# Optimization experiments

Hardware: AMD Instinct MI355X
Metric: run time of the kernel (lower is better)

Reference implementation:

```python
import jax, jax.numpy as jnp
import numpy as np

K = 20
EPS = 1e-5
N = 4096


def lrelu(x):
    return jnp.where(x >= 0, x, 0.2 * x)


def bn(x, g, b, m, v):
    # eval-mode BatchNorm over channel dim 1
    shape = [1] * x.ndim
    shape[1] = -1
    inv = g / jnp.sqrt(v + EPS)
    return (x - m.reshape(shape)) * inv.reshape(shape) + b.reshape(shape)


def get_graph_feature(x):
    # Faithful to repo: num_points = x.shape[1], remaining dims fold into channels.
    p = x.shape[1]
    x2d = x.reshape(-1, p)              # (C, P)
    xx = jnp.sum(x2d * x2d, axis=0)     # (P,)
    dist = 2.0 * (x2d.T @ x2d) - xx[:, None] - xx[None, :]  # -||xi-xj||^2, (P, P)
    idx = jax.lax.top_k(dist, K)[1]     # (P, K) nearest neighbors (incl. self)
    xt = x2d.T                          # (P, C)
    feat = xt[idx]                      # (P, K, C) neighbor gather
    ctr = jnp.broadcast_to(xt[:, None, :], feat.shape)
    out = jnp.concatenate([feat - ctr, ctr], axis=-1)  # (P, K, 2C)
    return out.transpose(2, 0, 1)[None]                # (1, 2C, P, K)


def setup_inputs():
    key = jax.random.key(0)
    ks = jax.random.split(key, 16)

    def w(k_, o, c):
        return jax.random.normal(k_, (o, c), jnp.float32) / float(np.sqrt(c))

    def bnp(k_, c):
        k1, k2, k3, k4 = jax.random.split(k_, 4)
        return (1.0 + 0.1 * jax.random.normal(k1, (c,), jnp.float32),
                0.1 * jax.random.normal(k2, (c,), jnp.float32),
                0.1 * jax.random.normal(k3, (c,), jnp.float32),
                jax.random.uniform(k4, (c,), jnp.float32, minval=0.5, maxval=1.5))

    g1, b1, m1, v1 = bnp(ks[1], 64)
    g2, b2, m2, v2 = bnp(ks[2], 64)
    g3, b3, m3, v3 = bnp(ks[3], 128)
    g4, b4, m4, v4 = bnp(ks[4], 256)
    g5, b5, m5, v5 = bnp(ks[5], 512)
    return dict(
        x=jax.random.normal(ks[0], (3, N), jnp.float32),
        w1=w(ks[6], 64, 6), g1=g1, b1=b1, m1=m1, v1=v1,
        w2=w(ks[7], 64, 64), g2=g2, b2=b2, m2=m2, v2=v2,
        w3=w(ks[8], 128, 64), g3=g3, b3=b3, m3=m3, v3=v3,
        w4=w(ks[9], 256, 128), g4=g4, b4=b4, m4=m4, v4=v4,
        w5=w(ks[10], 512, 256), g5=g5, b5=b5, m5=m5, v5=v5,
        lw1=w(ks[11], 512, 1024),
        lw2=w(ks[12], 256, 512),
        lb2=0.1 * jax.random.normal(ks[13], (256,), jnp.float32),
        ow=w(ks[14], 11, 256),
        ob=0.1 * jax.random.normal(ks[15], (11,), jnp.float32),
    )


def reference(x, w1, g1, b1, m1, v1, w2, g2, b2, m2, v2, w3, g3, b3, m3, v3,
              w4, g4, b4, m4, v4, w5, g5, b5, m5, v5, lw1, lw2, lb2, ow, ob):
    conv2d = lambda w_, f_: jnp.einsum('oc,bcpk->bopk', w_, f_)

    f = get_graph_feature(x)                                   # (1, 6, N, K)
    h = lrelu(bn(conv2d(w1, f), g1, b1, m1, v1))
    x1 = jnp.max(h, axis=-1)                                   # (1, 64, N)

    f = jnp.swapaxes(get_graph_feature(x1), 1, 2)              # (1, 64, 2N, K)
    h = lrelu(bn(conv2d(w2, f), g2, b2, m2, v2))
    x2 = jnp.max(h, axis=-1)                                   # (1, 64, 2N)

    f = jnp.swapaxes(get_graph_feature(x2), 1, 2)              # (1, 64, 4N, K)
    h = lrelu(bn(conv2d(w3, f), g3, b3, m3, v3))
    x3 = jnp.max(h, axis=-1)                                   # (1, 128, 4N)

    f = jnp.swapaxes(get_graph_feature(x3), 1, 2)              # (1, 128, 8N, K)
    h = lrelu(bn(conv2d(w4, f), g4, b4, m4, v4))
    x4 = jnp.max(h, axis=-1)                                   # (1, 256, 8N)

    h5 = lrelu(bn(jnp.einsum('oc,bcp->bop', w5, x4), g5, b5, m5, v5))  # (1, 512, 8N)
    pmax = jnp.max(h5, axis=-1)
    pavg = jnp.mean(h5, axis=-1)
    z = jnp.concatenate([pmax, pavg], axis=1)                  # (1, 1024)
    z = lrelu(z @ lw1.T)                                       # (1, 512); dropout = eval identity
    z = lrelu(z @ lw2.T + lb2)                                 # (1, 256)
    logits = z @ ow.T + ob                                     # (1, 11)
    return jax.nn.softmax(logits, axis=1)
```

## Files before the change

### kernel.cpp

```cpp
#include <hip/hip_runtime.h>
#include <hip/hip_bf16.h>
#include <float.h>
#include <math.h>

#define DEV __device__ __forceinline__

DEV float lrelu(float x) { return x >= 0.f ? x : 0.2f * x; }

constexpr int N = 4096, KNN = 20;

typedef __attribute__((ext_vector_type(4))) float f32x4;
typedef __attribute__((ext_vector_type(8))) short s16x8;

constexpr size_t OFF_SC1 = 0,    OFF_SH1 = 64;
constexpr size_t OFF_SC2 = 128,  OFF_SH2 = 192;
constexpr size_t OFF_SC3 = 256,  OFF_SH3 = 384;
constexpr size_t OFF_SC4 = 512,  OFF_SH4 = 768;
constexpr size_t OFF_SC5 = 1024, OFF_SH5 = 1536;
constexpr size_t OFF_X1 = 2048;
constexpr size_t OFF_X2 = OFF_X1 + (size_t)64*4096;
constexpr size_t OFF_X3 = OFF_X2 + (size_t)64*8192;
constexpr size_t OFF_X4 = OFF_X3 + (size_t)128*16384;
constexpr size_t OFF_A  = OFF_X4 + (size_t)256*32768;
constexpr size_t OFF_GP = OFF_A + (size_t)256*21*128;
constexpr size_t OFF_PM = OFF_GP + (size_t)64*128*128;
constexpr size_t OFF_PS = OFF_PM + (size_t)512*256;
constexpr size_t OFF_Z0 = OFF_PS + (size_t)512*256;
constexpr size_t OFF_Z1 = OFF_Z0 + 1024;
constexpr size_t OFF_Z2 = OFF_Z1 + 512;
constexpr size_t OFF_IDX = OFF_Z2 + 256;
constexpr size_t WS_NEEDED_BYTES = OFF_IDX * 4 + (size_t)N * KNN * 4;
constexpr size_t OFF_ABF = OFF_A;
constexpr size_t OFF_W5BF = OFF_A + 524288;

__global__ void k_ws_sentinel(float* out, float mb) {
  int t = threadIdx.x;
  if (t < 11) out[t] = 1.0e6f + mb;
}

__global__ __launch_bounds__(512) void k_bn_pre(
    const float* g1, const float* b1, const float* m1, const float* v1,
    const float* g2, const float* b2, const float* m2, const float* v2,
    const float* g3, const float* b3, const float* m3, const float* v3,
    const float* g4, const float* b4, const float* m4, const float* v4,
    const float* g5, const float* b5, const float* m5, const float* v5,
    float* ws) {
  int t = threadIdx.x;
  const float* G[5] = {g1,g2,g3,g4,g5};
  const float* B[5] = {b1,b2,b3,b4,b5};
  const float* M[5] = {m1,m2,m3,m4,m5};
  const float* V[5] = {v1,v2,v3,v4,v5};
  const size_t SC[5] = {OFF_SC1,OFF_SC2,OFF_SC3,OFF_SC4,OFF_SC5};
  const size_t SH[5] = {OFF_SH1,OFF_SH2,OFF_SH3,OFF_SH4,OFF_SH5};
  const int CN[5] = {64,64,128,256,512};
  for (int s = 0; s < 5; ++s) {
    for (int i = t; i < CN[s]; i += 512) {
      float scale = G[s][i] / sqrtf(V[s][i] + 1e-5f);
      ws[SC[s] + i] = scale;
      ws[SH[s] + i] = B[s][i] - M[s][i] * scale;
    }
  }
}

__global__ __launch_bounds__(256) void k_s1_topk(const float* x, int* idx) {
  __shared__ float d[N];
  __shared__ float vsh[256];
  __shared__ int ish[256];
  int i = blockIdx.x, t = threadIdx.x;
  {
    #pragma clang fp contract(off)
    float xi0 = x[i], xi1 = x[N + i], xi2 = x[2*N + i];
    float sqi = xi0*xi0 + xi1*xi1 + xi2*xi2;
    for (int j = t; j < N; j += 256) {
      float xj0 = x[j], xj1 = x[N+j], xj2 = x[2*N+j];
      float sqj = xj0*xj0 + xj1*xj1 + xj2*xj2;
      float p = xi0*xj0 + xi1*xj1 + xi2*xj2;
      d[j] = (2.f*p - sqi) - sqj;
    }
  }
  __syncthreads();
  for (int k = 0; k < KNN; ++k) {
    float bv = -FLT_MAX; int bi = N;
    for (int j = t; j < N; j += 256) { float v = d[j]; if (v > bv) { bv = v; bi = j; } }
    vsh[t] = bv; ish[t] = bi;
    __syncthreads();
    for (int s = 128; s > 0; s >>= 1) {
      if (t < s) {
        float v2 = vsh[t+s]; int i2 = ish[t+s];
        if (v2 > vsh[t] || (v2 == vsh[t] && i2 < ish[t])) { vsh[t] = v2; ish[t] = i2; }
      }
      __syncthreads();
    }
    if (t == 0) { idx[i*KNN + k] = ish[0]; d[ish[0]] = -FLT_MAX; }
    __syncthreads();
  }
}

__global__ __launch_bounds__(256) void k_s1_conv(const float* x, const float* w1g,
                                                 const int* idx, const float* sc, const float* sh, float* x1) {
  __shared__ int idxs[64][KNN];
  __shared__ float xs[3][64];
  __shared__ float wsh[4][6];
  int t = threadIdx.x, bx = blockIdx.x, by = blockIdx.y;
  int i0 = bx * 64;
  for (int u = t; u < 64*KNN; u += 256) idxs[u/KNN][u%KNN] = idx[(size_t)(i0 + u/KNN)*KNN + u%KNN];
  for (int u = t; u < 3*64; u += 256) xs[u/64][u%64] = x[(size_t)(u/64)*N + i0 + (u%64)];
  for (int u = t; u < 24; u += 256) wsh[u/6][u%6] = w1g[(size_t)(by*4 + u/6)*6 + u%6];
  __syncthreads();
  int il = t & 63, ol = t >> 6;
  int o = by*4 + ol, i = i0 + il;
  float xi0 = xs[0][il], xi1 = xs[1][il], xi2 = xs[2][il];
  float w0 = wsh[ol][0], w1v = wsh[ol][1], w2v = wsh[ol][2];
  float w3v = wsh[ol][3], w4v = wsh[ol][4], w5v = wsh[ol][5];
  float ctr = w3v*xi0 + w4v*xi1 + w5v*xi2;
  float scale = sc[o], shift = sh[o];
  float best = -FLT_MAX;
  for (int k = 0; k < KNN; ++k) {
    int j = idxs[il][k];
    float h = w0*(x[j] - xi0) + w1v*(x[N+j] - xi1) + w2v*(x[2*N+j] - xi2) + ctr;
    h = lrelu(h*scale + shift);
    best = fmaxf(best, h);
  }
  x1[(size_t)o*N + i] = best;
}

template<int P>
__global__ __launch_bounds__(256) void k_gram_partial(const float* prev, int C, float* gp) {
  constexpr int BI = P / 16;
  __shared__ float ysh[32][P];
  int b = blockIdx.x, t = threadIdx.x;
  int R = C / 64;
  int base = b * R;
  float acc[BI][BI] = {};
  int i0 = (t >> 4) * BI, j0 = (t & 15) * BI;
  for (int r0 = 0; r0 < R; r0 += 32) {
    for (int u = t; u < 32*P; u += 256) ysh[u/P][u%P] = prev[(size_t)(base + r0 + u/P)*P + (u%P)];
    __syncthreads();
    for (int r = 0; r < 32; ++r) {
      float yi[BI], yj[BI];
      #pragma unroll
      for (int a = 0; a < BI; ++a) { yi[a] = ysh[r][i0+a]; yj[a] = ysh[r][j0+a]; }
      #pragma unroll
      for (int a = 0; a < BI; ++a)
        #pragma unroll
        for (int c = 0; c < BI; ++c) acc[a][c] += yi[a]*yj[c];
    }
    __syncthreads();
  }
  for (int a = 0; a < BI; ++a)
    for (int c = 0; c < BI; ++c)
      gp[(size_t)b*P*P + (size_t)(i0+a)*P + (j0+c)] = acc[a][c];
}

template<int P>
__global__ __launch_bounds__(128) void k_dist_topk(const float* gp, int* idx) {
  __shared__ float dsh[P];
  __shared__ float diag[P];
  __shared__ float vsh[128];
  __shared__ int ish[128];
  int i = blockIdx.x, t = threadIdx.x;
  if (t < P) {
    float gij = 0.f, gjj = 0.f;
    for (int b = 0; b < 64; ++b) {
      gij += gp[(size_t)b*P*P + (size_t)i*P + t];
      gjj += gp[(size_t)b*P*P + (size_t)t*P + t];
    }
    diag[t] = gjj;
    dsh[t] = gij;
  }
  __syncthreads();
  if (t < P) dsh[t] = (2.f*dsh[t] - diag[i]) - diag[t];
  __syncthreads();
  for (int k = 0; k < KNN; ++k) {
    float bv = -FLT_MAX; int bi = P;
    if (t < P) { bv = dsh[t]; bi = t; }
    vsh[t] = bv; ish[t] = bi;
    __syncthreads();
    for (int s = 64; s > 0; s >>= 1) {
      if (t < s) {
        float v2 = vsh[t+s]; int i2 = ish[t+s];
        if (v2 > vsh[t] || (v2 == vsh[t] && i2 < ish[t])) { vsh[t] = v2; ish[t] = i2; }
      }
      __syncthreads();
    }
    if (t == 0) { idx[i*KNN + k] = ish[0]; dsh[ish[0]] = -FLT_MAX; }
    __syncthreads();
  }
}

template<int P>
__global__ __launch_bounds__(64) void k_build_A(const float* w, const int* idx, int O, float* A) {
  __shared__ float row[64][P];
  int t = threadIdx.x;
  int r = blockIdx.x*64 + t;
  if (r < O*21) {
    int o = r / 21, kk = r % 21;
    float* my = row[t];
    if (kk == 20) {
      for (int i2 = 0; i2 < P; ++i2) my[i2] = w[(size_t)o*P + i2];
    } else {
      for (int i2 = 0; i2 < P; ++i2) my[i2] = 0.f;
      for (int j = 0; j < P; ++j) my[idx[j*KNN + kk]] += w[(size_t)o*P + j];
    }
    for (int i2 = 0; i2 < P; ++i2) A[(size_t)r*P + i2] = my[i2];
  }
}

__global__ __launch_bounds__(64) void k_build_A_bf(const float* w, const int* idx, __hip_bfloat16* A) {
  __shared__ float row[64][128];
  int t = threadIdx.x;
  int r = blockIdx.x*64 + t;
  int o = r >> 5, kk = r & 31;
  float* my = row[t];
  if (kk == 20) {
    for (int i2 = 0; i2 < 128; ++i2) my[i2] = w[(size_t)o*128 + i2];
  } else if (kk < 20) {
    for (int i2 = 0; i2 < 128; ++i2) my[i2] = 0.f;
    for (int j = 0; j < 128; ++j) my[idx[j*KNN + kk]] += w[(size_t)o*128 + j];
  } else {
    for (int i2 = 0; i2 < 128; ++i2) my[i2] = 0.f;
  }
  for (int i2 = 0; i2 < 128; ++i2) A[(size_t)r*128 + i2] = __float2bfloat16(my[i2]);
}

__global__ __launch_bounds__(256) void k_f32_to_bf16(const float* in, __hip_bfloat16* out) {
  size_t base = ((size_t)blockIdx.x*256 + threadIdx.x) * 16;
  #pragma unroll
  for (int j = 0; j < 4; ++j) {
    float4 v = *(const float4*)(in + base + j*4);
    __hip_bfloat16 tmp[4] = {__float2bfloat16(v.x), __float2bfloat16(v.y),
                             __float2bfloat16(v.z), __float2bfloat16(v.w)};
    *(ushort4*)(out + base + j*4) = *(const ushort4*)tmp;
  }
}

__global__ __launch_bounds__(512, 2) void k_conv4_mfma(const __hip_bfloat16* Abf, const __hip_bfloat16* Xbf,
                                                       const float* sc, const float* sh, float* x4) {
  constexpr int MT = 256;
  __shared__ char Bs[MT*256];
  int t = threadIdx.x, bx = blockIdx.x, byg = blockIdx.y;
  int m0 = bx*MT;
  for (int u = t; u < MT*16; u += 512) {
    int row = u >> 4, k8 = u & 15;
    s16x8 v = *(const s16x8*)(Xbf + ((size_t)(m0+row) << 7) + (k8 << 3));
    *(s16x8*)(Bs + (row << 8) + ((k8 << 4) ^ ((row & 7) << 4))) = v;
  }
  __syncthreads();
  int lane = t & 63, w = t >> 6;
  int col = lane & 15, lg = lane >> 4;
  int q = w & 3, pb = w >> 2;
  for (int it = 0; it < 8; ++it) {
    int by = byg*16 + it*2 + pb;
    const __hip_bfloat16* Ab = Abf + ((size_t)(by*64) << 7);
    f32x4 acc[4][4] = {};
    #pragma unroll
    for (int ks = 0; ks < 4; ++ks) {
      int kel = ks*32 + lg*8;
      int kbyte = ks*64 + lg*16;
      s16x8 a[4], b[4];
      #pragma unroll
      for (int at = 0; at < 4; ++at)
        a[at] = *(const s16x8*)(Ab + ((size_t)(at*16 + col) << 7) + kel);
      #pragma unroll
      for (int bt = 0; bt < 4; ++bt) {
        int r = q*64 + bt*16 + col;
        b[bt] = *(const s16x8*)(Bs + (r << 8) + (kbyte ^ ((r & 7) << 4)));
      }
      #pragma unroll
      for (int at = 0; at < 4; ++at)
        #pragma unroll
        for (int bt = 0; bt < 4; ++bt)
          acc[at][bt] = __builtin_amdgcn_mfma_f32_16x16x32_bf16(a[at], b[bt], acc[at][bt], 0, 0, 0);
    }
    int o0 = by*2;
    #pragma unroll
    for (int ol = 0; ol < 2; ++ol) {
      float scale = sc[o0+ol], shift = sh[o0+ol];
      float mxv[4], ctv[4];
      #pragma unroll
      for (int bt = 0; bt < 4; ++bt) {
        float h2b = __shfl(acc[2*ol+1][bt][0], 16 + col);
        float mx = -FLT_MAX;
        #pragma unroll
        for (int qq = 0; qq < 4; ++qq) {
          mx = fmaxf(mx, lrelu((acc[2*ol][bt][qq] - h2b)*scale + shift));
          float v1 = lrelu((acc[2*ol+1][bt][qq] - h2b)*scale + shift);
          if (lg == 0) mx = fmaxf(mx, v1);
        }
        mx = fmaxf(mx, __shfl_xor(mx, 16));
        mx = fmaxf(mx, __shfl_xor(mx, 32));
        mxv[bt] = mx;
        ctv[bt] = lrelu(h2b*scale + shift);
      }
      float vb = (lg == 0) ? mxv[0] : (lg == 1) ? mxv[1] : (lg == 2) ? mxv[2] : mxv[3];
      float vc = (lg == 0) ? ctv[0] : (lg == 1) ? ctv[1] : (lg == 2) ? ctv[2] : ctv[3];
      size_t pbase = (size_t)(o0+ol)*32768 + m0 + q*64 + lane;
      x4[pbase] = vb;
      x4[pbase + 16384] = vc;
    }
  }
}

template<int P>
__global__ __launch_bounds__(256) void k_fused_conv(const float* prev, const float* A,
                                                    const float* sc, const float* sh,
                                                    int C, float* outx) {
  constexpr int TO = 8, ROWS = TO*21;
  __shared__ float Ash[ROWS][65];
  __shared__ float Bsh[64][132];
  int bx = blockIdx.x, by = blockIdx.y, t = threadIdx.x;
  int m0 = bx*128;
  int rowbase = by*ROWS;
  int ol = t >> 5, mg = t & 31;
  float acc[21][4] = {};
  for (int ic = 0; ic < P/64; ++ic) {
    for (int u = t; u < ROWS*64; u += 256) {
      int rr = u >> 6, cc = u & 63;
      Ash[rr][cc] = A[(size_t)(rowbase + rr)*P + ic*64 + cc];
    }
    for (int u = t; u < 64*128; u += 256) {
      int mr = u >> 6, ii = u & 63;
      Bsh[ii][mr] = prev[(size_t)(m0 + mr)*P + ic*64 + ii];
    }
    __syncthreads();
    for (int i = 0; i < 64; ++i) {
      float v0 = Bsh[i][mg*4+0], v1 = Bsh[i][mg*4+1], v2 = Bsh[i][mg*4+2], v3 = Bsh[i][mg*4+3];
      #pragma unroll
      for (int kk = 0; kk < 21; ++kk) {
        float a = Ash[ol*21 + kk][i];
        acc[kk][0] += a*v0; acc[kk][1] += a*v1; acc[kk][2] += a*v2; acc[kk][3] += a*v3;
      }
    }
    __syncthreads();
  }
  int o = by*TO + ol;
  float scale = sc[o], shift = sh[o];
  size_t C2 = 2*(size_t)C;
  #pragma unroll
  for (int mm = 0; mm < 4; ++mm) {
    int m = m0 + mg*4 + mm;
    float h2 = acc[20][mm];
    float ctr = lrelu(h2*scale + shift);
    float best = -FLT_MAX;
    #pragma unroll
    for (int kk = 0; kk < 20; ++kk) {
      float v = lrelu((acc[kk][mm] - h2)*scale + shift);
      best = fmaxf(best, v);
    }
    outx[(size_t)o*C2 + m] = best;
    outx[(size_t)o*C2 + C + m] = ctr;
  }
}

__global__ __launch_bounds__(256) void k_s5_mfma(const float* x4, const __hip_bfloat16* w5bf,
                                                 const float* sc, const float* sh,
                                                 float* pm, float* ps) {
  __shared__ char smem[8192 + 32768];
  __shared__ float redm[64][4];
  __shared__ float reds[64][4];
  int t = threadIdx.x, bx = blockIdx.x, by = blockIdx.y;
  int p0 = bx*256, o0 = by*64;
  int lane = t & 63, w = t >> 6;
  int lrow = lane & 15, lg = lane >> 4;
  char* As = smem;
  char* Bs = smem + 8192;
  f32x4 acc[4][4] = {};
  for (int c0 = 0; c0 < 256; c0 += 64) {
    for (int u = t; u < 64*8; u += 256) {
      int row = u >> 3, k8 = u & 7;
      s16x8 v = *(const s16x8*)(w5bf + (size_t)(o0+row)*256 + c0 + k8*8);
      *(s16x8*)(As + row*128 + ((k8*16) ^ ((row&7)<<4))) = v;
    }
    #pragma unroll
    for (int i = 0; i < 8; ++i) {
      __hip_bfloat16 tmp[8];
      #pragma unroll
      for (int j = 0; j < 8; ++j)
        tmp[j] = __float2bfloat16(x4[(size_t)(c0 + i*8 + j)*32768 + p0 + t]);
      *(s16x8*)(Bs + t*128 + ((i*16) ^ ((t&7)<<4))) = *(const s16x8*)tmp;
    }
    __syncthreads();
    #pragma unroll
    for (int ksub = 0; ksub < 2; ++ksub) {
      int kbyte = ksub*64 + lg*16;
      s16x8 a[4], b[4];
      #pragma unroll
      for (int rt = 0; rt < 4; ++rt) { int r = rt*16 + lrow; a[rt] = *(const s16x8*)(As + r*128 + (kbyte ^ ((r&7)<<4))); }
      #pragma unroll
      for (int cf = 0; cf < 4; ++cf) { int r = w*64 + cf*16 + lrow; b[cf] = *(const s16x8*)(Bs + r*128 + (kbyte ^ ((r&7)<<4))); }
      #pragma unroll
      for (int rt = 0; rt < 4; ++rt)
        #pragma unroll
        for (int cf = 0; cf < 4; ++cf)
          acc[rt][cf] = __builtin_amdgcn_mfma_f32_16x16x32_bf16(a[rt], b[cf], acc[rt][cf], 0, 0, 0);
    }
    __syncthreads();
  }
  #pragma unroll
  for (int rt = 0; rt < 4; ++rt) {
    #pragma unroll
    for (int q = 0; q < 4; ++q) {
      int ol = rt*16 + lg*4 + q;
      float scale = sc[o0+ol], shift = sh[o0+ol];
      float mx = -FLT_MAX, sm = 0.f;
      #pragma unroll
      for (int cf = 0; cf < 4; ++cf) {
        float h = lrelu(acc[rt][cf][q]*scale + shift);
        mx = fmaxf(mx, h); sm += h;
      }
      #pragma unroll
      for (int off2 = 1; off2 < 16; off2 <<= 1) {
        mx = fmaxf(mx, __shfl_xor(mx, off2));
        sm += __shfl_xor(sm, off2);
      }
      if (lrow == 0) { redm[ol][w] = mx; reds[ol][w] = sm; }
    }
  }
  __syncthreads();
  if (t < 64) {
    float mx = fmaxf(fmaxf(redm[t][0], redm[t][1]), fmaxf(redm[t][2], redm[t][3]));
    float sm = reds[t][0] + reds[t][1] + reds[t][2] + reds[t][3];
    pm[(size_t)(o0 + t)*128 + bx] = mx;
    ps[(size_t)(o0 + t)*128 + bx] = sm;
  }
}

__global__ __launch_bounds__(512) void k_pool(const float* pm, const float* ps, float* z0) {
  int t = threadIdx.x;
  for (int o = t; o < 512; o += 512) {
    float mx = -FLT_MAX, sm = 0.f;
    for (int nt = 0; nt < 128; ++nt) { mx = fmaxf(mx, pm[(size_t)o*128+nt]); sm += ps[(size_t)o*128+nt]; }
    z0[o] = mx;
    z0[512+o] = sm * (1.f/32768.f);
  }
}

__global__ __launch_bounds__(128) void k_fc1(const float* z0, const float* lw1, float* z1) {
  int bx = blockIdx.x, t = threadIdx.x;
  int rl = t >> 4, cl = t & 15;
  int r = bx*8 + rl;
  float acc = 0.f;
  for (int u = 0; u < 64; ++u) {
    int c = cl*64 + u;
    acc += z0[c] * lw1[(size_t)r*1024 + c];
  }
  #pragma unroll
  for (int off = 1; off < 16; off <<= 1) acc += __shfl_xor(acc, off);
  if (cl == 0) z1[r] = lrelu(acc);
}

__global__ __launch_bounds__(128) void k_fc2(const float* z1, const float* lw2,
                                             const float* lb2, float* z2) {
  int bx = blockIdx.x, t = threadIdx.x;
  int rl = t >> 4, cl = t & 15;
  int r = bx*8 + rl;
  float acc = 0.f;
  for (int u = 0; u < 32; ++u) {
    int c = cl*32 + u;
    acc += z1[c] * lw2[(size_t)r*512 + c];
  }
  #pragma unroll
  for (int off = 1; off < 16; off <<= 1) acc += __shfl_xor(acc, off);
  if (cl == 0) z2[r] = lrelu(acc + lb2[r]);
}

__global__ __launch_bounds__(64) void k_fc3(const float* z2, const float* ow,
                                            const float* ob, float* out) {
  __shared__ float lg[11];
  __shared__ float ex[11];
  int t = threadIdx.x;
  if (t < 11) {
    float acc = 0.f;
    for (int c = 0; c < 256; ++c) acc += z2[c] * ow[t*256 + c];
    lg[t] = acc + ob[t];
  }
  __syncthreads();
  if (t < 11) {
    float m = -FLT_MAX;
    for (int r = 0; r < 11; ++r) m = fmaxf(m, lg[r]);
    ex[t] = expf(lg[t] - m);
  }
  __syncthreads();
  if (t < 11) {
    float s = 0.f;
    for (int r = 0; r < 11; ++r) s += ex[r];
    out[t] = ex[t] / s;
  }
}

extern "C" void kernel_launch(void* const* d_in, const int* in_sizes, int n_in,
                              void* d_out, int out_size, void* d_ws, size_t ws_size,
                              hipStream_t stream) {
  auto f = [&](int i) { return (const float*)d_in[i]; };
  float* ws = (float*)d_ws;
  int* idx = (int*)(ws + OFF_IDX);
  float* out = (float*)d_out;

  if (ws_size < WS_NEEDED_BYTES) {
    k_ws_sentinel<<<1, 64, 0, stream>>>(out, (float)(ws_size >> 20));
    return;
  }

  __hip_bfloat16* Abf = (__hip_bfloat16*)(ws + OFF_ABF);
  __hip_bfloat16* Xbf = (__hip_bfloat16*)(ws + OFF_GP);
  __hip_bfloat16* w5bf = (__hip_bfloat16*)(ws + OFF_W5BF);
  float* x4 = ws + OFF_X4;

  k_bn_pre<<<1, 512, 0, stream>>>(f(2),f(3),f(4),f(5), f(7),f(8),f(9),f(10),
                                  f(12),f(13),f(14),f(15), f(17),f(18),f(19),f(20),
                                  f(22),f(23),f(24),f(25), ws);
  k_s1_topk<<<N, 256, 0, stream>>>(f(0), idx);
  k_s1_conv<<<dim3(N/64, 16), 256, 0, stream>>>(f(0), f(1), idx, ws+OFF_SC1, ws+OFF_SH1, ws+OFF_X1);
  k_gram_partial<64><<<64, 256, 0, stream>>>(ws+OFF_X1, 4096, ws+OFF_GP);
  k_dist_topk<64><<<64, 128, 0, stream>>>(ws+OFF_GP, idx);
  k_build_A<64><<<21, 64, 0, stream>>>(f(6), idx, 64, ws+OFF_A);
  k_fused_conv<64><<<dim3(4096/128, 64/8), 256, 0, stream>>>(ws+OFF_X1, ws+OFF_A, ws+OFF_SC2, ws+OFF_SH2, 4096, ws+OFF_X2);
  k_gram_partial<64><<<64, 256, 0, stream>>>(ws+OFF_X2, 8192, ws+OFF_GP);
  k_dist_topk<64><<<64, 128, 0, stream>>>(ws+OFF_GP, idx);
  k_build_A<64><<<42, 64, 0, stream>>>(f(11), idx, 128, ws+OFF_A);
  k_fused_conv<64><<<dim3(8192/128, 128/8), 256, 0, stream>>>(ws+OFF_X2, ws+OFF_A, ws+OFF_SC3, ws+OFF_SH3, 8192, ws+OFF_X3);
  k_gram_partial<128><<<64, 256, 0, stream>>>(ws+OFF_X3, 16384, ws+OFF_GP);
  k_dist_topk<128><<<128, 128, 0, stream>>>(ws+OFF_GP, idx);
  k_build_A_bf<<<128, 64, 0, stream>>>(f(16), idx, Abf);
  k_f32_to_bf16<<<512, 256, 0, stream>>>(ws+OFF_X3, Xbf);
  k_conv4_mfma<<<dim3(16384/256, 8), 512, 0, stream>>>(Abf, Xbf, ws+OFF_SC4, ws+OFF_SH4, x4);
  k_f32_to_bf16<<<32, 256, 0, stream>>>(f(21), w5bf);
  k_s5_mfma<<<dim3(128, 8), 256, 0, stream>>>(x4, w5bf, ws+OFF_SC5, ws+OFF_SH5, ws+OFF_PM, ws+OFF_PS);
  k_pool<<<1, 512, 0, stream>>>(ws+OFF_PM, ws+OFF_PS, ws+OFF_Z0);
  k_fc1<<<64, 128, 0, stream>>>(ws+OFF_Z0, f(26), ws+OFF_Z1);
  k_fc2<<<32, 128, 0, stream>>>(ws+OFF_Z1, f(27), f(28), ws+OFF_Z2);
  k_fc3<<<1, 64, 0, stream>>>(ws+OFF_Z2, f(29), f(30), out);
}
```

Baseline: 504.4 us.

## Use wave-shuffle incremental top-k in stage 1 and split gram partials finer

The stage-1 top-k now keeps each thread's local best across iterations, reduces it with wave shuffles plus a 4-entry shared combine instead of a shared-memory tree, and rescans only in the thread that owned the selected index. The gram partial kernels launch 128-256 blocks instead of 64 to use more CUs, and the distance kernel sums the matching number of partials. The stage-4 partials are written into the x4 buffer to fit the larger size. This trades more partial-sum reads in the distance kernel and depends on x4 being free at that point.

```diff
diff --git a/kernel.cpp b/kernel.cpp
--- a/kernel.cpp
+++ b/kernel.cpp
@@ -64,8 +64,8 @@
 
 __global__ __launch_bounds__(256) void k_s1_topk(const float* x, int* idx) {
   __shared__ float d[N];
-  __shared__ float vsh[256];
-  __shared__ int ish[256];
+  __shared__ float wls[4];
+  __shared__ int wis[4];
   int i = blockIdx.x, t = threadIdx.x;
   {
     #pragma clang fp contract(off)
@@ -79,19 +79,30 @@
     }
   }
   __syncthreads();
+  int lane = t & 63, wid = t >> 6;
+  float bv = -FLT_MAX; int bi = N;
+  for (int j = t; j < N; j += 256) { float v = d[j]; if (v > bv) { bv = v; bi = j; } }
   for (int k = 0; k < KNN; ++k) {
-    float bv = -FLT_MAX; int bi = N;
-    for (int j = t; j < N; j += 256) { float v = d[j]; if (v > bv) { bv = v; bi = j; } }
-    vsh[t] = bv; ish[t] = bi;
-    __syncthreads();
-    for (int s = 128; s > 0; s >>= 1) {
-      if (t < s) {
-        float v2 = vsh[t+s]; int i2 = ish[t+s];
-        if (v2 > vsh[t] || (v2 == vsh[t] && i2 < ish[t])) { vsh[t] = v2; ish[t] = i2; }
-      }
-      __syncthreads();
-    }
-    if (t == 0) { idx[i*KNN + k] = ish[0]; d[ish[0]] = -FLT_MAX; }
+    float rv = bv; int ri = bi;
+    #pragma unroll
+    for (int off = 1; off < 64; off <<= 1) {
+      float v2 = __shfl_xor(rv, off); int i2 = __shfl_xor(ri, off);
+      if (v2 > rv || (v2 == rv && i2 < ri)) { rv = v2; ri = i2; }
+    }
+    if (lane == 0) { wls[wid] = rv; wis[wid] = ri; }
+    __syncthreads();
+    float fv = wls[0]; int fi = wis[0];
+    #pragma unroll
+    for (int w2 = 1; w2 < 4; ++w2) {
+      float v2 = wls[w2]; int i2 = wis[w2];
+      if (v2 > fv || (v2 == fv && i2 < fi)) { fv = v2; fi = i2; }
+    }
+    if (t == 0) idx[i*KNN + k] = fi;
+    if ((fi & 255) == t) {
+      d[fi] = -FLT_MAX;
+      bv = -FLT_MAX; bi = N;
+      for (int j = t; j < N; j += 256) { float v = d[j]; if (v > bv) { bv = v; bi = j; } }
+    }
     __syncthreads();
   }
 }
@@ -129,7 +140,7 @@
   constexpr int BI = P / 16;
   __shared__ float ysh[32][P];
   int b = blockIdx.x, t = threadIdx.x;
-  int R = C / 64;
+  int R = C / gridDim.x;
   int base = b * R;
   float acc[BI][BI] = {};
   int i0 = (t >> 4) * BI, j0 = (t & 15) * BI;
@@ -153,7 +164,7 @@
 }
 
 template<int P>
-__global__ __launch_bounds__(128) void k_dist_topk(const float* gp, int* idx) {
+__global__ __launch_bounds__(128) void k_dist_topk(const float* gp, int* idx, int nb) {
   __shared__ float dsh[P];
   __shared__ float diag[P];
   __shared__ float vsh[128];
@@ -161,7 +172,7 @@
   int i = blockIdx.x, t = threadIdx.x;
   if (t < P) {
     float gij = 0.f, gjj = 0.f;
-    for (int b = 0; b < 64; ++b) {
+    for (int b = 0; b < nb; ++b) {
       gij += gp[(size_t)b*P*P + (size_t)i*P + t];
       gjj += gp[(size_t)b*P*P + (size_t)t*P + t];
     }
@@ -511,16 +522,16 @@
                                   f(22),f(23),f(24),f(25), ws);
   k_s1_topk<<<N, 256, 0, stream>>>(f(0), idx);
   k_s1_conv<<<dim3(N/64, 16), 256, 0, stream>>>(f(0), f(1), idx, ws+OFF_SC1, ws+OFF_SH1, ws+OFF_X1);
-  k_gram_partial<64><<<64, 256, 0, stream>>>(ws+OFF_X1, 4096, ws+OFF_GP);
-  k_dist_topk<64><<<64, 128, 0, stream>>>(ws+OFF_GP, idx);
+  k_gram_partial<64><<<128, 256, 0, stream>>>(ws+OFF_X1, 4096, ws+OFF_GP);
+  k_dist_topk<64><<<64, 128, 0, stream>>>(ws+OFF_GP, idx, 128);
   k_build_A<64><<<21, 64, 0, stream>>>(f(6), idx, 64, ws+OFF_A);
   k_fused_conv<64><<<dim3(4096/128, 64/8), 256, 0, stream>>>(ws+OFF_X1, ws+OFF_A, ws+OFF_SC2, ws+OFF_SH2, 4096, ws+OFF_X2);
-  k_gram_partial<64><<<64, 256, 0, stream>>>(ws+OFF_X2, 8192, ws+OFF_GP);
-  k_dist_topk<64><<<64, 128, 0, stream>>>(ws+OFF_GP, idx);
+  k_gram_partial<64><<<256, 256, 0, stream>>>(ws+OFF_X2, 8192, ws+OFF_GP);
+  k_dist_topk<64><<<64, 128, 0, stream>>>(ws+OFF_GP, idx, 256);
   k_build_A<64><<<42, 64, 0, stream>>>(f(11), idx, 128, ws+OFF_A);
   k_fused_conv<64><<<dim3(8192/128, 128/8), 256, 0, stream>>>(ws+OFF_X2, ws+OFF_A, ws+OFF_SC3, ws+OFF_SH3, 8192, ws+OFF_X3);
-  k_gram_partial<128><<<64, 256, 0, stream>>>(ws+OFF_X3, 16384, ws+OFF_GP);
-  k_dist_topk<128><<<128, 128, 0, stream>>>(ws+OFF_GP, idx);
+  k_gram_partial<128><<<256, 256, 0, stream>>>(ws+OFF_X3, 16384, x4);
+  k_dist_topk<128><<<128, 128, 0, stream>>>(x4, idx, 256);
   k_build_A_bf<<<128, 64, 0, stream>>>(f(16), idx, Abf);
   k_f32_to_bf16<<<512, 256, 0, stream>>>(ws+OFF_X3, Xbf);
   k_conv4_mfma<<<dim3(16384/256, 8), 512, 0, stream>>>(Abf, Xbf, ws+OFF_SC4, ws+OFF_SH4, x4);
```

Measured after the change: 653.6 us. 29.6% more time.
